# Kernel optimization log

Measured on AMD Instinct MI355X. Metric: run time of the kernel, lower is better.

The kernel has to match this reference:

```python
import jax, jax.numpy as jnp
import numpy as np

D, H, HKV, HD = 1024, 16, 4, 64
ROPE_BASE = 10000.0
QK_GAIN_INIT = 1.0


def setup_inputs() -> dict:
    key = jax.random.key(0)
    ks = jax.random.split(key, 6)
    B, S = 2, 2048
    kv_dim = HKV * HD
    x = jax.random.normal(ks[0], (B, S, D), dtype=jnp.float32)
    Wq = jax.random.normal(ks[1], (D, D), dtype=jnp.float32) * 0.02
    Wk = jax.random.normal(ks[2], (kv_dim, D), dtype=jnp.float32) * 0.02
    Wv = jax.random.normal(ks[3], (kv_dim, D), dtype=jnp.float32) * 0.02
    Wo = jax.random.normal(ks[4], (D, D), dtype=jnp.float32) * 0.02
    q_gain = jnp.full((H,), QK_GAIN_INIT, dtype=jnp.float32)
    return {"x": x, "Wq": Wq, "Wk": Wk, "Wv": Wv, "Wo": Wo, "q_gain": q_gain}


def _rms_norm(t):
    eps = jnp.finfo(t.dtype).eps
    return t * jax.lax.rsqrt(jnp.mean(t * t, axis=-1, keepdims=True) + eps)


def _rope(t, cos, sin):
    # t: [B,h,S,HD]; cos/sin: [1,1,S,HD//2]
    half = t.shape[-1] // 2
    t1, t2 = t[..., :half], t[..., half:]
    return jnp.concatenate((t1 * cos + t2 * sin, -t1 * sin + t2 * cos), axis=-1)


def _attention(x, Wq, Wk, Wv, Wo, q_gain):
    B, S, _ = x.shape
    q = (x @ Wq.T).reshape(B, S, H, HD).transpose(0, 2, 1, 3)     # [B,H,S,HD]
    k = (x @ Wk.T).reshape(B, S, HKV, HD).transpose(0, 2, 1, 3)   # [B,HKV,S,HD]
    v = (x @ Wv.T).reshape(B, S, HKV, HD).transpose(0, 2, 1, 3)
    q, k = _rms_norm(q), _rms_norm(k)
    # rotary tables
    inv_freq = 1.0 / (ROPE_BASE ** (jnp.arange(0, HD, 2, dtype=jnp.float32) / HD))
    freqs = jnp.arange(S, dtype=jnp.float32)[:, None] * inv_freq[None, :]  # [S,HD//2]
    cos, sin = jnp.cos(freqs)[None, None], jnp.sin(freqs)[None, None]
    q, k = _rope(q, cos, sin), _rope(k, cos, sin)
    q = q * q_gain[None, :, None, None]
    # GQA: repeat kv heads to match query heads
    g = H // HKV
    k = jnp.repeat(k, g, axis=1)
    v = jnp.repeat(v, g, axis=1)
    scale = 1.0 / jnp.sqrt(jnp.asarray(HD, q.dtype))
    scores = jnp.einsum('bhqd,bhkd->bhqk', q, k) * scale
    causal = jnp.tril(jnp.ones((S, S), dtype=bool))
    scores = jnp.where(causal[None, None], scores, jnp.asarray(-jnp.inf, scores.dtype))
    attn = jax.nn.softmax(scores, axis=-1)
    y = jnp.einsum('bhqk,bhkd->bhqd', attn, v)                    # [B,H,S,HD]
    y = y.transpose(0, 2, 1, 3).reshape(B, S, D)
    return y @ Wo.T


def reference(x, Wq, Wk, Wv, Wo, q_gain):
    return _attention(x, Wq, Wk, Wv, Wo, q_gain)
```

## Files before the change

### kernel.cpp

```cpp
#include <hip/hip_runtime.h>
#include <hip/hip_bf16.h>
#include <math.h>

typedef __attribute__((ext_vector_type(8))) __bf16 bf16x8;
typedef __attribute__((ext_vector_type(4))) short short4v;
typedef __attribute__((ext_vector_type(4))) float f32x4;
typedef __attribute__((ext_vector_type(4))) unsigned short ushort4v;
typedef __attribute__((ext_vector_type(8))) unsigned short ushort8;

#define LOG2E 1.44269504088896340736f

static __device__ __forceinline__ unsigned short f2bf(float f) {
  unsigned int u = __float_as_uint(f);
  return (unsigned short)((u + 0x7fffu + ((u >> 16) & 1u)) >> 16);
}
static __device__ __forceinline__ short bfbits(float f) {
  __bf16 h = (__bf16)f;
  return __builtin_bit_cast(short, h);
}
static __device__ __forceinline__ float bf2f(unsigned short u) {
  unsigned int v = ((unsigned int)u) << 16;
  return __builtin_bit_cast(float, v);
}

static __device__ __forceinline__ void gload16(const unsigned short* g, void* l) {
  __builtin_amdgcn_global_load_lds(
      (const __attribute__((address_space(1))) unsigned int*)g,
      (__attribute__((address_space(3))) unsigned int*)l, 16, 0, 0);
}

__global__ __launch_bounds__(256) void prep_kernel(
    const float* __restrict__ x, const float* __restrict__ Wq,
    const float* __restrict__ Wk, const float* __restrict__ Wv,
    const float* __restrict__ Wo,
    unsigned short* __restrict__ xb, unsigned short* __restrict__ wqkv,
    unsigned short* __restrict__ wo_b, float* __restrict__ tab) {
  const int bx = blockIdx.x, tid = threadIdx.x;
  if (bx < 6656) {
    const float* src;
    unsigned short* dst;
    int i;
    if (bx < 4096)       { src = x;  dst = xb;             i = bx * 256 + tid; }
    else if (bx < 5120)  { src = Wq; dst = wqkv;           i = (bx - 4096) * 256 + tid; }
    else if (bx < 5376)  { src = Wk; dst = wqkv + 1048576; i = (bx - 5120) * 256 + tid; }
    else if (bx < 5632)  { src = Wv; dst = wqkv + 1310720; i = (bx - 5376) * 256 + tid; }
    else                 { src = Wo; dst = wo_b;           i = (bx - 5632) * 256 + tid; }
    float4 v = reinterpret_cast<const float4*>(src)[i];
    ushort4v o;
    o.x = f2bf(v.x); o.y = f2bf(v.y); o.z = f2bf(v.z); o.w = f2bf(v.w);
    reinterpret_cast<ushort4v*>(dst)[i] = o;
  } else {
    int i = (bx - 6656) * 256 + tid;
    int s = i >> 5, d = i & 31;
    float invf = powf(10000.f, -(float)d / 32.f);
    float fr = (float)s * invf;
    tab[s * 64 + d] = cosf(fr);
    tab[s * 64 + 32 + d] = sinf(fr);
  }
}

template <bool B16OUT>
__global__ __launch_bounds__(256) void gemm_bt_kernel(
    const unsigned short* __restrict__ A, const unsigned short* __restrict__ B,
    void* __restrict__ Cv, int M, int N, int K, int nbn) {
  __shared__ unsigned short sA[64 * 64];
  __shared__ unsigned short sB[128 * 64];
  const int t = threadIdx.x;
  const int lane = t & 63;
  const int w = t >> 6;
  const int bm = blockIdx.x / nbn, bn = blockIdx.x % nbn;
  const long m0 = (long)bm * 64, n0 = (long)bn * 128;
  const int wm = (w >> 1) * 32, wn = (w & 1) * 64;
  const int lr = lane & 15, lg = lane >> 4;
  f32x4 acc[2][4];
#pragma unroll
  for (int i = 0; i < 2; i++)
#pragma unroll
    for (int j = 0; j < 4; j++) acc[i][j] = (f32x4){0.f, 0.f, 0.f, 0.f};

  for (int k0 = 0; k0 < K; k0 += 64) {
#pragma unroll
    for (int i = 0; i < 2; i++) {
      int chunk = i * 256 + t;
      int r = chunk >> 3;
      int c = (chunk & 7) << 3;
      gload16(A + (m0 + r) * (long)K + k0 + c, (char*)sA + chunk * 16);
    }
#pragma unroll
    for (int i = 0; i < 4; i++) {
      int chunk = i * 256 + t;
      int r = chunk >> 3;
      int c = (chunk & 7) << 3;
      gload16(B + (n0 + r) * (long)K + k0 + c, (char*)sB + chunk * 16);
    }
    __syncthreads();
#pragma unroll
    for (int kk = 0; kk < 2; ++kk) {
      bf16x8 af[2], bfr[4];
#pragma unroll
      for (int m = 0; m < 2; m++)
        af[m] = *(const bf16x8*)&sA[(wm + m * 16 + lr) * 64 + kk * 32 + lg * 8];
#pragma unroll
      for (int n = 0; n < 4; n++)
        bfr[n] = *(const bf16x8*)&sB[(wn + n * 16 + lr) * 64 + kk * 32 + lg * 8];
#pragma unroll
      for (int m = 0; m < 2; m++)
#pragma unroll
        for (int n = 0; n < 4; n++)
          acc[m][n] = __builtin_amdgcn_mfma_f32_16x16x32_bf16(af[m], bfr[n], acc[m][n], 0, 0, 0);
    }
    __syncthreads();
  }
#pragma unroll
  for (int m = 0; m < 2; m++) {
#pragma unroll
    for (int n = 0; n < 4; n++) {
      long col = n0 + wn + n * 16 + lr;
#pragma unroll
      for (int j = 0; j < 4; j++) {
        long row = m0 + wm + m * 16 + lg * 4 + j;
        if (B16OUT)
          ((unsigned short*)Cv)[row * N + col] = f2bf(acc[m][n][j]);
        else
          ((float*)Cv)[row * N + col] = acc[m][n][j];
      }
    }
  }
}

__global__ __launch_bounds__(256) void pack_kernel(
    const unsigned short* __restrict__ qkv, const float* __restrict__ tab,
    const float* __restrict__ qg,
    unsigned short* __restrict__ qb, unsigned short* __restrict__ kb) {
  const int wid = (blockIdx.x * 256 + threadIdx.x) >> 6;
  const int lane = threadIdx.x & 63;
  const int row = wid / 20;
  const int u = wid % 20;
  const int b = row >> 11, s = row & 2047;
  float v;
  if (u < 16) v = bf2f(qkv[(size_t)row * 1536 + u * 64 + lane]);
  else        v = bf2f(qkv[(size_t)row * 1536 + 1024 + (u - 16) * 64 + lane]);
  float ss = v * v;
#pragma unroll
  for (int m = 32; m >= 1; m >>= 1) ss += __shfl_xor(ss, m);
  float n = v * rsqrtf(ss * (1.0f / 64.0f) + 1.1920929e-07f);
  int i = lane & 31;
  float c = tab[s * 64 + i], sn = tab[s * 64 + 32 + i];
  float p = __shfl_xor(n, 32);
  float o = (lane < 32) ? (n * c + p * sn) : (n * c - p * sn);
  if (u < 16) {
    o *= qg[u] * (0.125f * LOG2E);
    qb[((size_t)(b * 16 + u) * 2048 + s) * 64 + lane] = f2bf(o);
  } else {
    kb[((size_t)(b * 4 + (u - 16)) * 2048 + s) * 64 + lane] = f2bf(o);
  }
}

__global__ __launch_bounds__(256) void vpack_kernel(
    const unsigned short* __restrict__ qkv, unsigned short* __restrict__ vtb) {
  __shared__ unsigned short sT[64 * 65];
  const int tid = threadIdx.x;
  const int bhk = blockIdx.x >> 5;
  const int st = blockIdx.x & 31;
  const int b = bhk >> 2, hk = bhk & 3;
  const int r = tid >> 2, cg = (tid & 3) << 4;
  const unsigned short* src = qkv + (size_t)(b * 2048 + st * 64 + r) * 1536 + 1280 + hk * 64 + cg;
  ushort8 v0 = *(const ushort8*)src;
  ushort8 v1 = *(const ushort8*)(src + 8);
#pragma unroll
  for (int k = 0; k < 8; ++k) sT[r * 65 + cg + k] = v0[k];
#pragma unroll
  for (int k = 0; k < 8; ++k) sT[r * 65 + cg + 8 + k] = v1[k];
  __syncthreads();
  const int d = tid >> 2, sg = (tid & 3) << 4;
  ushort8 o0, o1;
#pragma unroll
  for (int k = 0; k < 8; ++k) o0[k] = sT[(sg + k) * 65 + d];
#pragma unroll
  for (int k = 0; k < 8; ++k) o1[k] = sT[(sg + 8 + k) * 65 + d];
  unsigned short* dst = vtb + ((size_t)(bhk * 64 + d)) * 2048 + st * 64 + sg;
  *(ushort8*)dst = o0;
  *(ushort8*)(dst + 8) = o1;
}

__global__ __launch_bounds__(256) void attn_kernel(
    const unsigned short* __restrict__ qb, const unsigned short* __restrict__ kb,
    const unsigned short* __restrict__ vtb, unsigned short* __restrict__ yb,
    const float* __restrict__ qg) {
  __shared__ unsigned short sK[2][64 * 64];
  __shared__ unsigned short sV[2][64 * 64];
  const int tid = threadIdx.x;
  const int lane = tid & 63;
  const int w = tid >> 6;
  const int qt = 31 - (blockIdx.x >> 5);
  const int bh = blockIdx.x & 31;
  const int h = bh & 15;
  const int b = bh >> 4;
  const float M = 11.7f * fabsf(qg[h]);
  const int q0 = qt * 64 + w * 16;
  const unsigned short* Q  = qb  + (size_t)(b * 16 + h) * 2048 * 64;
  const unsigned short* Kp = kb  + (size_t)(b * 4 + (h >> 2)) * 2048 * 64;
  const unsigned short* Vp = vtb + (size_t)(b * 4 + (h >> 2)) * 64 * 2048;
  const int qc = lane & 15;
  const int g = lane >> 4;
  const int qrow = q0 + qc;
  const bf16x8 qf0 = *(const bf16x8*)(Q + (size_t)qrow * 64 + g * 8);
  const bf16x8 qf1 = *(const bf16x8*)(Q + (size_t)qrow * 64 + 32 + g * 8);
  f32x4 acc[4];
  acc[0] = acc[1] = acc[2] = acc[3] = (f32x4){0.f, 0.f, 0.f, 0.f};
  float lsum = 0.f;
  const int nt = qt + 1;

  const int r0 = tid >> 3, c0 = tid & 7;
  const int swz = ((c0 ^ (r0 & 7)) << 3);
  const unsigned short* gK = Kp + (size_t)r0 * 64 + swz;
  const unsigned short* gV = Vp + (size_t)r0 * 2048 + swz;

  gload16(gK,             (char*)&sK[0][0] + tid * 16);
  gload16(gK + 32 * 64,   (char*)&sK[0][0] + (tid + 256) * 16);
  gload16(gV,             (char*)&sV[0][0] + tid * 16);
  gload16(gV + 32 * 2048, (char*)&sV[0][0] + (tid + 256) * 16);
  gK += 64 * 64; gV += 64;

  int cur = 0;
  for (int t = 0; t < nt; ++t) {
    __syncthreads();
    if (t + 1 < nt) {
      const int nb = cur ^ 1;
      gload16(gK,             (char*)&sK[nb][0] + tid * 16);
      gload16(gK + 32 * 64,   (char*)&sK[nb][0] + (tid + 256) * 16);
      gload16(gV,             (char*)&sV[nb][0] + tid * 16);
      gload16(gV + 32 * 2048, (char*)&sV[nb][0] + (tid + 256) * 16);
      gK += 64 * 64; gV += 64;
    }
    const unsigned short* sKc = &sK[cur][0];
    const unsigned short* sVc = &sV[cur][0];
    f32x4 st[4];
    __builtin_amdgcn_s_setprio(1);
#pragma unroll
    for (int ks = 0; ks < 4; ++ks) {
      const int rr = ks * 16 + qc;
      bf16x8 kf0 = *(const bf16x8*)&sKc[rr * 64 + ((g ^ (rr & 7)) << 3)];
      bf16x8 kf1 = *(const bf16x8*)&sKc[rr * 64 + (((4 + g) ^ (rr & 7)) << 3)];
      f32x4 a = (f32x4){0.f, 0.f, 0.f, 0.f};
      a = __builtin_amdgcn_mfma_f32_16x16x32_bf16(kf0, qf0, a, 0, 0, 0);
      a = __builtin_amdgcn_mfma_f32_16x16x32_bf16(kf1, qf1, a, 0, 0, 0);
      st[ks] = a;
    }
    __builtin_amdgcn_s_setprio(0);
    if (t == nt - 1) {
#pragma unroll
      for (int ks = 0; ks < 4; ++ks)
#pragma unroll
        for (int j = 0; j < 4; ++j)
          if (ks * 16 + g * 4 + j > w * 16 + qc) st[ks][j] = -1e30f;
    }
    short4v pb[4];
#pragma unroll
    for (int ks = 0; ks < 4; ++ks)
#pragma unroll
      for (int j = 0; j < 4; ++j) {
        float p = exp2f(st[ks][j] - M);
        lsum += p;
        pb[ks][j] = bfbits(p);
      }
    __builtin_amdgcn_s_setprio(1);
#pragma unroll
    for (int ks = 0; ks < 4; ++ks) {
#pragma unroll
      for (int d = 0; d < 4; ++d) {
        const int rd = d * 16 + qc;
        const int el = rd * 64 + ((((ks * 2 + (g >> 1)) ^ (rd & 7)) << 3) + ((g & 1) << 2));
        short4v vf = *(const short4v*)&sVc[el];
        acc[d] = __builtin_amdgcn_mfma_f32_16x16x16bf16_1k(vf, pb[ks], acc[d], 0, 0, 0);
      }
    }
    __builtin_amdgcn_s_setprio(0);
    cur ^= 1;
  }
  float l = lsum;
  l += __shfl_xor(l, 16);
  l += __shfl_xor(l, 32);
  const float inv = 1.0f / l;
  unsigned short* Y = yb + (size_t)(b * 2048 + qrow) * 1024 + h * 64;
#pragma unroll
  for (int d = 0; d < 4; ++d)
#pragma unroll
    for (int j = 0; j < 4; ++j)
      Y[d * 16 + g * 4 + j] = (unsigned short)bfbits(acc[d][j] * inv);
}

extern "C" void kernel_launch(void* const* d_in, const int* in_sizes, int n_in,
                              void* d_out, int out_size, void* d_ws, size_t ws_size,
                              hipStream_t stream) {
  const float* x  = (const float*)d_in[0];
  const float* Wq = (const float*)d_in[1];
  const float* Wk = (const float*)d_in[2];
  const float* Wv = (const float*)d_in[3];
  const float* Wo = (const float*)d_in[4];
  const float* qg = (const float*)d_in[5];
  float* out = (float*)d_out;

  char* ws = (char*)d_ws;
  const size_t NEED = 47710208;
  if (ws_size < NEED) return;
  unsigned short* xb   = (unsigned short*)(ws);
  unsigned short* wqkv = (unsigned short*)(ws + 8388608);
  unsigned short* wo_b = (unsigned short*)(ws + 11534336);
  unsigned short* qkvb = (unsigned short*)(ws + 13631488);
  unsigned short* qbuf = (unsigned short*)(ws + 26214400);
  unsigned short* kbuf = (unsigned short*)(ws + 34603008);
  unsigned short* vtb  = (unsigned short*)(ws + 36700160);
  unsigned short* ybuf = (unsigned short*)(ws + 38797312);
  float*          tab  = (float*)        (ws + 47185920);

  prep_kernel<<<6912, 256, 0, stream>>>(x, Wq, Wk, Wv, Wo, xb, wqkv, wo_b, tab);
  gemm_bt_kernel<true><<<64 * 12, 256, 0, stream>>>(xb, wqkv, qkvb, 4096, 1536, 1024, 12);
  pack_kernel<<<20480, 256, 0, stream>>>(qkvb, tab, qg, qbuf, kbuf);
  vpack_kernel<<<256, 256, 0, stream>>>(qkvb, vtb);
  attn_kernel<<<1024, 256, 0, stream>>>(qbuf, kbuf, vtb, ybuf, qg);
  gemm_bt_kernel<false><<<64 * 8, 256, 0, stream>>>(ybuf, wo_b, out, 4096, 1024, 1024, 8);
}
```

Before: 119.7 us.

## Fuse RMSNorm, RoPE and q-gain into the QKV GEMM epilogue

The QKV projection GEMM now applies per-head RMS normalization, rotary embedding and q-gain scaling in its epilogue and writes Q and K directly in head-major bf16 layout. V goes to a compact slab that the transpose kernel reads. This removes the separate pack kernel and the round trip of the full QKV intermediate through global memory. In exchange the epilogue does cross-lane shuffles and scattered 2-byte stores, which may raise GEMM epilogue cost.

```diff
diff --git a/kernel.cpp b/kernel.cpp
--- a/kernel.cpp
+++ b/kernel.cpp
@@ -17,10 +17,6 @@
 static __device__ __forceinline__ short bfbits(float f) {
   __bf16 h = (__bf16)f;
   return __builtin_bit_cast(short, h);
-}
-static __device__ __forceinline__ float bf2f(unsigned short u) {
-  unsigned int v = ((unsigned int)u) << 16;
-  return __builtin_bit_cast(float, v);
 }
 
 static __device__ __forceinline__ void gload16(const unsigned short* g, void* l) {
@@ -59,10 +55,116 @@
   }
 }
 
-template <bool B16OUT>
+__global__ __launch_bounds__(256) void gemm_qkv_kernel(
+    const unsigned short* __restrict__ A, const unsigned short* __restrict__ B,
+    const float* __restrict__ tab, const float* __restrict__ qg,
+    unsigned short* __restrict__ qb, unsigned short* __restrict__ kb,
+    unsigned short* __restrict__ vsl) {
+  __shared__ unsigned short sA[64 * 64];
+  __shared__ unsigned short sB[128 * 64];
+  const int t = threadIdx.x;
+  const int lane = t & 63;
+  const int w = t >> 6;
+  const int bm = blockIdx.x / 12, bn = blockIdx.x % 12;
+  const long m0 = (long)bm * 64, n0 = (long)bn * 128;
+  const int wm = (w >> 1) * 32, wn = (w & 1) * 64;
+  const int lr = lane & 15, lg = lane >> 4;
+  f32x4 acc[2][4];
+#pragma unroll
+  for (int i = 0; i < 2; i++)
+#pragma unroll
+    for (int j = 0; j < 4; j++) acc[i][j] = (f32x4){0.f, 0.f, 0.f, 0.f};
+
+  for (int k0 = 0; k0 < 1024; k0 += 64) {
+#pragma unroll
+    for (int i = 0; i < 2; i++) {
+      int chunk = i * 256 + t;
+      int r = chunk >> 3;
+      int c = (chunk & 7) << 3;
+      gload16(A + (m0 + r) * 1024 + k0 + c, (char*)sA + chunk * 16);
+    }
+#pragma unroll
+    for (int i = 0; i < 4; i++) {
+      int chunk = i * 256 + t;
+      int r = chunk >> 3;
+      int c = (chunk & 7) << 3;
+      gload16(B + (n0 + r) * 1024 + k0 + c, (char*)sB + chunk * 16);
+    }
+    __syncthreads();
+#pragma unroll
+    for (int kk = 0; kk < 2; ++kk) {
+      bf16x8 af[2], bfr[4];
+#pragma unroll
+      for (int m = 0; m < 2; m++)
+        af[m] = *(const bf16x8*)&sA[(wm + m * 16 + lr) * 64 + kk * 32 + lg * 8];
+#pragma unroll
+      for (int n = 0; n < 4; n++)
+        bfr[n] = *(const bf16x8*)&sB[(wn + n * 16 + lr) * 64 + kk * 32 + lg * 8];
+#pragma unroll
+      for (int m = 0; m < 2; m++)
+#pragma unroll
+        for (int n = 0; n < 4; n++)
+          acc[m][n] = __builtin_amdgcn_mfma_f32_16x16x32_bf16(af[m], bfr[n], acc[m][n], 0, 0, 0);
+    }
+    __syncthreads();
+  }
+  const int bb = (int)(m0 >> 11);
+  const int s_base = (int)(m0 & 2047) + wm + lg * 4;
+  const int hsel = wn >> 6;
+  if (bn < 10) {
+    float gscale = 1.0f;
+    unsigned short* dstb;
+    if (bn < 8) {
+      gscale = qg[2 * bn + hsel] * (0.125f * LOG2E);
+      dstb = qb + (size_t)(bb * 16 + 2 * bn + hsel) * 2048 * 64;
+    } else {
+      dstb = kb + (size_t)(bb * 4 + 2 * (bn - 8) + hsel) * 2048 * 64;
+    }
+#pragma unroll
+    for (int m = 0; m < 2; m++) {
+#pragma unroll
+      for (int j = 0; j < 4; j++) {
+        float ss = acc[m][0][j] * acc[m][0][j] + acc[m][1][j] * acc[m][1][j] +
+                   acc[m][2][j] * acc[m][2][j] + acc[m][3][j] * acc[m][3][j];
+        ss += __shfl_xor(ss, 1);
+        ss += __shfl_xor(ss, 2);
+        ss += __shfl_xor(ss, 4);
+        ss += __shfl_xor(ss, 8);
+        const float rinv = rsqrtf(ss * (1.0f / 64.0f) + 1.1920929e-07f);
+        const int s = s_base + m * 16 + j;
+        const float* tr = tab + s * 64;
+        const float c0 = tr[lr], c1 = tr[16 + lr];
+        const float s0 = tr[32 + lr], s1 = tr[48 + lr];
+        const float n0v = acc[m][0][j] * rinv, n1v = acc[m][1][j] * rinv;
+        const float n2v = acc[m][2][j] * rinv, n3v = acc[m][3][j] * rinv;
+        float o0 = (n0v * c0 + n2v * s0) * gscale;
+        float o1 = (n1v * c1 + n3v * s1) * gscale;
+        float o2 = (n2v * c0 - n0v * s0) * gscale;
+        float o3 = (n3v * c1 - n1v * s1) * gscale;
+        unsigned short* d = dstb + (size_t)s * 64;
+        d[lr]      = f2bf(o0);
+        d[16 + lr] = f2bf(o1);
+        d[32 + lr] = f2bf(o2);
+        d[48 + lr] = f2bf(o3);
+      }
+    }
+  } else {
+#pragma unroll
+    for (int m = 0; m < 2; m++) {
+#pragma unroll
+      for (int j = 0; j < 4; j++) {
+        const int s = s_base + m * 16 + j;
+        unsigned short* d = vsl + (size_t)(bb * 2048 + s) * 256 + (bn - 10) * 128 + wn;
+#pragma unroll
+        for (int n = 0; n < 4; n++) d[n * 16 + lr] = f2bf(acc[m][n][j]);
+      }
+    }
+  }
+}
+
 __global__ __launch_bounds__(256) void gemm_bt_kernel(
     const unsigned short* __restrict__ A, const unsigned short* __restrict__ B,
-    void* __restrict__ Cv, int M, int N, int K, int nbn) {
+    float* __restrict__ C, int M, int N, int K, int nbn) {
   __shared__ unsigned short sA[64 * 64];
   __shared__ unsigned short sB[128 * 64];
   const int t = threadIdx.x;
@@ -119,52 +221,21 @@
 #pragma unroll
       for (int j = 0; j < 4; j++) {
         long row = m0 + wm + m * 16 + lg * 4 + j;
-        if (B16OUT)
-          ((unsigned short*)Cv)[row * N + col] = f2bf(acc[m][n][j]);
-        else
-          ((float*)Cv)[row * N + col] = acc[m][n][j];
-      }
-    }
-  }
-}
-
-__global__ __launch_bounds__(256) void pack_kernel(
-    const unsigned short* __restrict__ qkv, const float* __restrict__ tab,
-    const float* __restrict__ qg,
-    unsigned short* __restrict__ qb, unsigned short* __restrict__ kb) {
-  const int wid = (blockIdx.x * 256 + threadIdx.x) >> 6;
-  const int lane = threadIdx.x & 63;
-  const int row = wid / 20;
-  const int u = wid % 20;
-  const int b = row >> 11, s = row & 2047;
-  float v;
-  if (u < 16) v = bf2f(qkv[(size_t)row * 1536 + u * 64 + lane]);
-  else        v = bf2f(qkv[(size_t)row * 1536 + 1024 + (u - 16) * 64 + lane]);
-  float ss = v * v;
-#pragma unroll
-  for (int m = 32; m >= 1; m >>= 1) ss += __shfl_xor(ss, m);
-  float n = v * rsqrtf(ss * (1.0f / 64.0f) + 1.1920929e-07f);
-  int i = lane & 31;
-  float c = tab[s * 64 + i], sn = tab[s * 64 + 32 + i];
-  float p = __shfl_xor(n, 32);
-  float o = (lane < 32) ? (n * c + p * sn) : (n * c - p * sn);
-  if (u < 16) {
-    o *= qg[u] * (0.125f * LOG2E);
-    qb[((size_t)(b * 16 + u) * 2048 + s) * 64 + lane] = f2bf(o);
-  } else {
-    kb[((size_t)(b * 4 + (u - 16)) * 2048 + s) * 64 + lane] = f2bf(o);
+        C[row * N + col] = acc[m][n][j];
+      }
+    }
   }
 }
 
 __global__ __launch_bounds__(256) void vpack_kernel(
-    const unsigned short* __restrict__ qkv, unsigned short* __restrict__ vtb) {
+    const unsigned short* __restrict__ vsl, unsigned short* __restrict__ vtb) {
   __shared__ unsigned short sT[64 * 65];
   const int tid = threadIdx.x;
   const int bhk = blockIdx.x >> 5;
   const int st = blockIdx.x & 31;
   const int b = bhk >> 2, hk = bhk & 3;
   const int r = tid >> 2, cg = (tid & 3) << 4;
-  const unsigned short* src = qkv + (size_t)(b * 2048 + st * 64 + r) * 1536 + 1280 + hk * 64 + cg;
+  const unsigned short* src = vsl + (size_t)(b * 2048 + st * 64 + r) * 256 + hk * 64 + cg;
   ushort8 v0 = *(const ushort8*)src;
   ushort8 v1 = *(const ushort8*)(src + 8);
 #pragma unroll
@@ -302,22 +373,21 @@
   float* out = (float*)d_out;
 
   char* ws = (char*)d_ws;
-  const size_t NEED = 47710208;
+  const size_t NEED = 37224448;
   if (ws_size < NEED) return;
   unsigned short* xb   = (unsigned short*)(ws);
   unsigned short* wqkv = (unsigned short*)(ws + 8388608);
   unsigned short* wo_b = (unsigned short*)(ws + 11534336);
-  unsigned short* qkvb = (unsigned short*)(ws + 13631488);
-  unsigned short* qbuf = (unsigned short*)(ws + 26214400);
-  unsigned short* kbuf = (unsigned short*)(ws + 34603008);
-  unsigned short* vtb  = (unsigned short*)(ws + 36700160);
-  unsigned short* ybuf = (unsigned short*)(ws + 38797312);
-  float*          tab  = (float*)        (ws + 47185920);
+  unsigned short* vsl  = (unsigned short*)(ws + 13631488);
+  unsigned short* qbuf = (unsigned short*)(ws + 15728640);
+  unsigned short* kbuf = (unsigned short*)(ws + 24117248);
+  unsigned short* vtb  = (unsigned short*)(ws + 26214400);
+  unsigned short* ybuf = (unsigned short*)(ws + 28311552);
+  float*          tab  = (float*)        (ws + 36700160);
 
   prep_kernel<<<6912, 256, 0, stream>>>(x, Wq, Wk, Wv, Wo, xb, wqkv, wo_b, tab);
-  gemm_bt_kernel<true><<<64 * 12, 256, 0, stream>>>(xb, wqkv, qkvb, 4096, 1536, 1024, 12);
-  pack_kernel<<<20480, 256, 0, stream>>>(qkvb, tab, qg, qbuf, kbuf);
-  vpack_kernel<<<256, 256, 0, stream>>>(qkvb, vtb);
+  gemm_qkv_kernel<<<64 * 12, 256, 0, stream>>>(xb, wqkv, tab, qg, qbuf, kbuf, vsl);
+  vpack_kernel<<<256, 256, 0, stream>>>(vsl, vtb);
   attn_kernel<<<1024, 256, 0, stream>>>(qbuf, kbuf, vtb, ybuf, qg);
-  gemm_bt_kernel<false><<<64 * 8, 256, 0, stream>>>(ybuf, wo_b, out, 4096, 1024, 1024, 8);
-}
+  gemm_bt_kernel<<<64 * 8, 256, 0, stream>>>(ybuf, wo_b, out, 4096, 1024, 1024, 8);
+}
```

Measured after the change: 108.0 us. -9.8%, faster.
